# Optimization experiments

Hardware: AMD Instinct MI355X
Metric: run time of the kernel (lower is better)

## Reference

```python
import jax, jax.numpy as jnp
import numpy as np

N_NODES = 50000
N_GRAPHS = 500
E_SPARSE = 800000
E_DENSE = 3200000
IN_DIM = 128
HID = 128          # nb_hidden
OUT = HID // 2     # per-branch GATConv output
N_LAYERS = 3
NEG_SLOPE = 0.2    # PyG GATConv default


def setup_inputs() -> dict:
    key = jax.random.key(0)
    ks = jax.random.split(key, 10)
    x = jax.random.normal(ks[0], (N_NODES, IN_DIM), dtype=jnp.float32)
    edge_index = jax.random.randint(ks[1], (2, E_SPARSE), 0, N_NODES, dtype=jnp.int32)
    dense_edge_idx = jax.random.randint(ks[2], (2, E_DENSE), 0, N_NODES, dtype=jnp.int32)
    batch = jnp.sort(jax.random.randint(ks[3], (N_NODES,), 0, N_GRAPHS, dtype=jnp.int32))
    # One weight set per layer (source code aliases layersB = layersA, so both
    # branches share weights). All layers have in_dim = 128 -> out = 64.
    lin_w = jax.random.normal(ks[4], (N_LAYERS, HID, OUT), dtype=jnp.float32) * 0.1
    att_src = jax.random.normal(ks[5], (N_LAYERS, OUT), dtype=jnp.float32) * 0.1
    att_dst = jax.random.normal(ks[6], (N_LAYERS, OUT), dtype=jnp.float32) * 0.1
    bias = jnp.zeros((N_LAYERS, OUT), dtype=jnp.float32)
    final_w = jax.random.normal(ks[7], (HID, 1), dtype=jnp.float32) * 0.1
    final_b = jnp.zeros((1,), dtype=jnp.float32)
    return {"x": x, "edge_index": edge_index, "dense_edge_idx": dense_edge_idx,
            "batch": batch, "lin_w": lin_w, "att_src": att_src,
            "att_dst": att_dst, "bias": bias, "final_w": final_w,
            "final_b": final_b}


def _with_self_loops(edge_index, n):
    loop = jnp.arange(n, dtype=edge_index.dtype)
    src = jnp.concatenate([edge_index[0], loop])
    dst = jnp.concatenate([edge_index[1], loop])
    return src, dst


def _gat(x, src, dst, W, a_s, a_d, b):
    """PyG GATConv, heads=1: gather, LeakyReLU attention, segment softmax over
    incoming edges of each dst node, scatter-add aggregation."""
    n = x.shape[0]
    h = x @ W                      # [N, OUT]
    s_src = h @ a_s                # [N] per-node source score
    s_dst = h @ a_d                # [N] per-node dest score
    e = jax.nn.leaky_relu(s_src[src] + s_dst[dst], NEG_SLOPE)  # [E]
    m = jax.ops.segment_max(e, dst, num_segments=n)
    p = jnp.exp(e - m[dst])
    z = jax.ops.segment_sum(p, dst, num_segments=n)
    alpha = p / z[dst]             # [E] softmax over neighbors of dst
    out = jax.ops.segment_sum(alpha[:, None] * h[src], dst, num_segments=n)
    return out + b


def reference(x, edge_index, dense_edge_idx, batch, lin_w, att_src, att_dst,
              bias, final_w, final_b):
    n = x.shape[0]
    srcA, dstA = _with_self_loops(edge_index, n)
    srcB, dstB = _with_self_loops(dense_edge_idx, n)
    for l in range(N_LAYERS):
        xA = _gat(x, srcA, dstA, lin_w[l], att_src[l], att_dst[l], bias[l])
        xB = _gat(x, srcB, dstB, lin_w[l], att_src[l], att_dst[l], bias[l])
        x = jax.nn.relu(jnp.concatenate([xA, xB], axis=1))
    g = jax.ops.segment_sum(x, batch, num_segments=N_GRAPHS)  # global_add_pool
    y = (g @ final_w + final_b).squeeze()
    return y
```

## Files before the change

### kernel.cpp

```cpp
#include <hip/hip_runtime.h>
#include <hip/hip_fp16.h>

#define N_NODES 50000
#define N_GRAPHS 500
#define E_SPARSE 800000
#define E_DENSE 3200000
#define IN_DIM 128
#define HID 128
#define OUT_D 64
#define N_LAYERS 3
#define NEG_SLOPE 0.2f

#define BUCKET_SHIFT 7
#define BUCKET_N 128
#define NBUCK 391
#define NTD 256
#define NTS 64
#define TS_D 12500
#define TS_S 12500
#define MD (NBUCK * NTD)
#define MATN (NBUCK * (NTD + NTS))
#define NT 32
typedef unsigned int u32;
typedef unsigned short u16;
typedef _Float16 h16x8 __attribute__((ext_vector_type(8)));


__global__ __launch_bounds__(256) void tile_count_all(
    const int* __restrict__ dstD, const int* __restrict__ dstS,
    int* __restrict__ mat) {
    __shared__ int hc[NBUCK];
    int t = threadIdx.x;
    int tile = blockIdx.x;
    for (int i = t; i < NBUCK; i += 256) hc[i] = 0;
    __syncthreads();
    if (tile < NTD) {
        int beg = tile * TS_D, end = min(E_DENSE, beg + TS_D);
        for (int i = beg + t; i < end; i += 256)
            atomicAdd(&hc[dstD[i] >> BUCKET_SHIFT], 1);
        __syncthreads();
        for (int i = t; i < NBUCK; i += 256) mat[i * NTD + tile] = hc[i];
    } else {
        int st = tile - NTD;
        int beg = st * TS_S, end = min(E_SPARSE, beg + TS_S);
        for (int i = beg + t; i < end; i += 256)
            atomicAdd(&hc[dstS[i] >> BUCKET_SHIFT], 1);
        __syncthreads();
        for (int i = t; i < NBUCK; i += 256) mat[MD + i * NTS + st] = hc[i];
    }
}

__global__ void scan_lvl0(const int* __restrict__ cnt, int n,
                          int* __restrict__ out, int* __restrict__ bsum) {
    __shared__ int sm[512];
    int t = threadIdx.x;
    int base = blockIdx.x * 2048 + t * 4;
    int v0 = (base + 0 < n) ? cnt[base + 0] : 0;
    int v1 = (base + 1 < n) ? cnt[base + 1] : 0;
    int v2 = (base + 2 < n) ? cnt[base + 2] : 0;
    int v3 = (base + 3 < n) ? cnt[base + 3] : 0;
    int s = v0 + v1 + v2 + v3;
    sm[t] = s;
    __syncthreads();
    for (int off = 1; off < 512; off <<= 1) {
        int a = (t >= off) ? sm[t - off] : 0;
        __syncthreads();
        sm[t] += a;
        __syncthreads();
    }
    int excl = sm[t] - s;
    if (base + 0 < n) out[base + 0] = excl;
    if (base + 1 < n) out[base + 1] = excl + v0;
    if (base + 2 < n) out[base + 2] = excl + v0 + v1;
    if (base + 3 < n) out[base + 3] = excl + v0 + v1 + v2;
    if (t == 511) bsum[blockIdx.x] = sm[511];
}

__global__ void scan_lvl1(const int* __restrict__ bsum, int nb,
                          int* __restrict__ bsumx) {
    __shared__ int sm[256];
    int t = threadIdx.x;
    int v = (t < nb) ? bsum[t] : 0;
    sm[t] = v;
    __syncthreads();
    for (int off = 1; off < 256; off <<= 1) {
        int a = (t >= off) ? sm[t - off] : 0;
        __syncthreads();
        sm[t] += a;
        __syncthreads();
    }
    if (t < nb) bsumx[t] = sm[t] - v;
}

__global__ void scan_add(int* __restrict__ out, int n, const int* __restrict__ bsumx,
                         int Etot) {
    int i = blockIdx.x * blockDim.x + threadIdx.x;
    if (i < n) out[i] += bsumx[i >> 11];
    if (i == 0) out[n] = Etot;
}

__global__ __launch_bounds__(256) void tile_scatter_all(
    const int* __restrict__ srcD, const int* __restrict__ dstD,
    const int* __restrict__ srcS, const int* __restrict__ dstS,
    const int* __restrict__ matx, u32* __restrict__ pairs) {
    __shared__ int cur[NBUCK];
    int t = threadIdx.x;
    int tile = blockIdx.x;
    const int* src;
    const int* dst;
    int beg, end;
    if (tile < NTD) {
        for (int i = t; i < NBUCK; i += 256) cur[i] = matx[i * NTD + tile];
        src = srcD; dst = dstD;
        beg = tile * TS_D; end = min(E_DENSE, beg + TS_D);
    } else {
        int st = tile - NTD;
        for (int i = t; i < NBUCK; i += 256) cur[i] = matx[MD + i * NTS + st];
        src = srcS; dst = dstS;
        beg = st * TS_S; end = min(E_SPARSE, beg + TS_S);
    }
    __syncthreads();
    for (int i = beg + t; i < end; i += 256) {
        int d = dst[i];
        int pos = atomicAdd(&cur[d >> BUCKET_SHIFT], 1);
        pairs[pos] = (u32)src[i] | ((u32)(d & (BUCKET_N - 1)) << 16);
    }
}

__global__ __launch_bounds__(256) void bucket_to_csr_all(
    const u32* __restrict__ pairs, const int* __restrict__ matx,
    int* __restrict__ rowD, u16* __restrict__ csrcD,
    int* __restrict__ rowS, u16* __restrict__ csrcS) {
    int bid = blockIdx.x;
    int t = threadIdx.x;
    int b, beg, end, base;
    int* rowptr;
    u16* csrc;
    if (bid < NBUCK) {
        b = bid;
        beg = matx[b * NTD];
        end = matx[(b + 1) * NTD];
        base = 0; rowptr = rowD; csrc = csrcD;
    } else {
        b = bid - NBUCK;
        beg = matx[MD + b * NTS];
        end = matx[MD + (b + 1) * NTS];
        base = E_DENSE; rowptr = rowS; csrc = csrcS;
    }
    __shared__ int lcnt[BUCKET_N];
    __shared__ int lofs[BUCKET_N];
    if (t < BUCKET_N) lcnt[t] = 0;
    __syncthreads();
    for (int k = beg + t; k < end; k += 256)
        atomicAdd(&lcnt[(pairs[k] >> 16) & (BUCKET_N - 1)], 1);
    __syncthreads();
    if (t < BUCKET_N) lofs[t] = lcnt[t];
    __syncthreads();
    for (int off = 1; off < BUCKET_N; off <<= 1) {
        int a = (t < BUCKET_N && t >= off) ? lofs[t - off] : 0;
        __syncthreads();
        if (t < BUCKET_N) lofs[t] += a;
        __syncthreads();
    }
    int node = (b << BUCKET_SHIFT) + t;
    int lbeg = beg - base;
    if (t < BUCKET_N) {
        int excl = lofs[t] - lcnt[t];
        if (node < N_NODES) rowptr[node] = lbeg + excl;
        lcnt[t] = excl;
    }
    if (b == NBUCK - 1 && t == 0)
        rowptr[N_NODES] = (base == 0) ? E_DENSE : E_SPARSE;
    __syncthreads();
    for (int k = beg + t; k < end; k += 256) {
        u32 pr = pairs[k];
        int dl = (pr >> 16) & (BUCKET_N - 1);
        int pos = atomicAdd(&lcnt[dl], 1);
        csrc[lbeg + pos] = (u16)(pr & 0xffffu);
    }
}


__global__ __launch_bounds__(256) void node_mm2(
    const float* __restrict__ x, const float* __restrict__ W,
    const float* __restrict__ a_s, const float* __restrict__ a_d,
    __half* __restrict__ h, float* __restrict__ s_src, float* __restrict__ s_dst) {
    __shared__ float Wl[IN_DIM * OUT_D];
    __shared__ float4 Xl4[NT * 33];
    int t = threadIdx.x;
    int nbase = blockIdx.x * NT;

    const float4* W4 = (const float4*)W;
    float4* Wl4 = (float4*)Wl;
#pragma unroll
    for (int i = 0; i < 8; ++i) Wl4[t + 256 * i] = W4[t + 256 * i];

    int nrows = min(NT, N_NODES - nbase);
    const float4* X4 = (const float4*)(x + (size_t)nbase * IN_DIM);
    for (int i = t; i < nrows * 32; i += 256)
        Xl4[(i >> 5) * 33 + (i & 31)] = X4[i];
    __syncthreads();

    int wv = t >> 6, l = t & 63;
    int c4 = l & 15;
    int np = l >> 4;
    int n0 = wv * 8 + np * 2, n1 = n0 + 1;
    const float* Xl = (const float*)Xl4;
    const float4* Wr = (const float4*)Wl;

    float4 A0 = make_float4(0.f, 0.f, 0.f, 0.f);
    float4 A1 = make_float4(0.f, 0.f, 0.f, 0.f);
#pragma unroll 4
    for (int k = 0; k < IN_DIM; ++k) {
        float4 w4 = Wr[k * 16 + c4];
        float x0 = Xl[n0 * 132 + k];
        float x1 = Xl[n1 * 132 + k];
        A0.x += x0 * w4.x; A0.y += x0 * w4.y; A0.z += x0 * w4.z; A0.w += x0 * w4.w;
        A1.x += x1 * w4.x; A1.y += x1 * w4.y; A1.z += x1 * w4.z; A1.w += x1 * w4.w;
    }
    int gn0 = nbase + n0, gn1 = nbase + n1;
    if (gn0 < N_NODES) {
        __half2 v0 = __floats2half2_rn(A0.x, A0.y);
        __half2 v1 = __floats2half2_rn(A0.z, A0.w);
        float2 pk;
        pk.x = *(float*)&v0; pk.y = *(float*)&v1;
        ((float2*)(h + (size_t)gn0 * OUT_D))[c4] = pk;
    }
    if (gn1 < N_NODES) {
        __half2 v0 = __floats2half2_rn(A1.x, A1.y);
        __half2 v1 = __floats2half2_rn(A1.z, A1.w);
        float2 pk;
        pk.x = *(float*)&v0; pk.y = *(float*)&v1;
        ((float2*)(h + (size_t)gn1 * OUT_D))[c4] = pk;
    }

    float4 as4 = ((const float4*)a_s)[c4];
    float4 ad4 = ((const float4*)a_d)[c4];
    float ps0 = A0.x * as4.x + A0.y * as4.y + A0.z * as4.z + A0.w * as4.w;
    float pd0 = A0.x * ad4.x + A0.y * ad4.y + A0.z * ad4.z + A0.w * ad4.w;
    float ps1 = A1.x * as4.x + A1.y * as4.y + A1.z * as4.z + A1.w * as4.w;
    float pd1 = A1.x * ad4.x + A1.y * ad4.y + A1.z * ad4.z + A1.w * ad4.w;
#pragma unroll
    for (int off = 1; off < 16; off <<= 1) {
        ps0 += __shfl_xor(ps0, off); pd0 += __shfl_xor(pd0, off);
        ps1 += __shfl_xor(ps1, off); pd1 += __shfl_xor(pd1, off);
    }
    if (c4 == 0) {
        if (gn0 < N_NODES) { s_src[gn0] = ps0; s_dst[gn0] = pd0; }
        if (gn1 < N_NODES) { s_src[gn1] = ps1; s_dst[gn1] = pd1; }
    }
}

__device__ __forceinline__ void accv(float4& a0, float4& a1, float p,
                                     const h16x8& r) {
    a0.x = fmaf((float)r[0], p, a0.x);
    a0.y = fmaf((float)r[1], p, a0.y);
    a0.z = fmaf((float)r[2], p, a0.z);
    a0.w = fmaf((float)r[3], p, a0.w);
    a1.x = fmaf((float)r[4], p, a1.x);
    a1.y = fmaf((float)r[5], p, a1.y);
    a1.z = fmaf((float)r[6], p, a1.z);
    a1.w = fmaf((float)r[7], p, a1.w);
}

__device__ __forceinline__ float lrelu(float e) {
    return (e >= 0.f) ? e : NEG_SLOPE * e;
}

__global__ __launch_bounds__(256, 8) void gat_aggr2(
    const int* __restrict__ rowS, const u16* __restrict__ csrcS,
    const int* __restrict__ rowD, const u16* __restrict__ csrcD,
    const float* __restrict__ s_src, const float* __restrict__ s_dst,
    const __half* __restrict__ h, const float* __restrict__ bias,
    float* __restrict__ xnext, int ngrid) {
    int bid = blockIdx.x;
    const int* rowptr;
    const u16* csrc;
    int col_off;
    if (bid < ngrid) { rowptr = rowS; csrc = csrcS; col_off = 0; }
    else { bid -= ngrid; rowptr = rowD; csrc = csrcD; col_off = OUT_D; }

    int node = bid * 4 + (threadIdx.x >> 6);
    if (node >= N_NODES) return;
    int lane = threadIdx.x & 63;
    int grp = lane >> 3;
    int sub = lane & 7;

    int beg = rowptr[node];
    int end = rowptr[node + 1];
    float sd = s_dst[node];

    const char* hb = (const char*)h;
    u32 subo = (u32)sub * 16u;

    float4 a0 = make_float4(0.f, 0.f, 0.f, 0.f);
    float4 a1 = make_float4(0.f, 0.f, 0.f, 0.f);
    float zb = 0.f;
    float zt = 0.f;

    int kb = beg;
    for (; kb + 32 <= end; kb += 32) {
        u32 idx = csrc[kb + (lane & 31)];
        float e = s_src[idx] + sd;
        float p = __expf(lrelu(e));
        if (lane < 32) zb += p;
#pragma unroll
        for (int i = 0; i < 4; ++i) {
            int j = (grp << 2) + i;
            float pj = __shfl(p, j);
            u32 ij = (u32)__shfl((int)idx, j);
            h16x8 r = *(const h16x8*)(hb + (ij * 128u + subo));
            accv(a0, a1, pj, r);
        }
    }
    int k = kb + grp;
    for (; k + 8 < end; k += 16) {
        u32 s0 = csrc[k], s1 = csrc[k + 8];
        h16x8 r0 = *(const h16x8*)(hb + (s0 * 128u + subo));
        h16x8 r1 = *(const h16x8*)(hb + (s1 * 128u + subo));
        float e0 = s_src[s0] + sd;
        float e1 = s_src[s1] + sd;
        float p0 = __expf(lrelu(e0));
        float p1 = __expf(lrelu(e1));
        zt += p0 + p1;
        accv(a0, a1, p0, r0);
        accv(a0, a1, p1, r1);
    }
    if (k < end) {
        u32 s0 = csrc[k];
        h16x8 r0 = *(const h16x8*)(hb + (s0 * 128u + subo));
        float e0 = s_src[s0] + sd;
        float p0 = __expf(lrelu(e0));
        zt += p0;
        accv(a0, a1, p0, r0);
    }
    if (grp == 0) {
        h16x8 r0 = *(const h16x8*)(hb + ((u32)node * 128u + subo));
        float e0 = s_src[node] + sd;
        float p0 = __expf(lrelu(e0));
        zt += p0;
        accv(a0, a1, p0, r0);
    }
#pragma unroll
    for (int off = 1; off <= 32; off <<= 1) zb += __shfl_xor(zb, off);
#pragma unroll
    for (int off = 8; off <= 32; off <<= 1) {
        a0.x += __shfl_xor(a0.x, off); a0.y += __shfl_xor(a0.y, off);
        a0.z += __shfl_xor(a0.z, off); a0.w += __shfl_xor(a0.w, off);
        a1.x += __shfl_xor(a1.x, off); a1.y += __shfl_xor(a1.y, off);
        a1.z += __shfl_xor(a1.z, off); a1.w += __shfl_xor(a1.w, off);
        zt += __shfl_xor(zt, off);
    }
    if (grp == 0) {
        float inv = 1.f / (zb + zt);
        const float4* b4 = (const float4*)bias;
        float4 b0 = b4[sub * 2], b1 = b4[sub * 2 + 1];
        float4 o0, o1;
        o0.x = a0.x * inv + b0.x; o0.y = a0.y * inv + b0.y;
        o0.z = a0.z * inv + b0.z; o0.w = a0.w * inv + b0.w;
        o1.x = a1.x * inv + b1.x; o1.y = a1.y * inv + b1.y;
        o1.z = a1.z * inv + b1.z; o1.w = a1.w * inv + b1.w;
        o0.x = fmaxf(o0.x, 0.f); o0.y = fmaxf(o0.y, 0.f);
        o0.z = fmaxf(o0.z, 0.f); o0.w = fmaxf(o0.w, 0.f);
        o1.x = fmaxf(o1.x, 0.f); o1.y = fmaxf(o1.y, 0.f);
        o1.z = fmaxf(o1.z, 0.f); o1.w = fmaxf(o1.w, 0.f);
        float4* outp = (float4*)(xnext + (size_t)node * HID + col_off);
        outp[sub * 2] = o0;
        outp[sub * 2 + 1] = o1;
    }
}

__global__ __launch_bounds__(128) void pool_final(
    const float* __restrict__ x, const int* __restrict__ batch,
    const float* __restrict__ fw, const float* __restrict__ fb,
    float* __restrict__ y) {
    int b = blockIdx.x;
    int t = threadIdx.x;
    __shared__ int sbeg, send;
    if (t == 0) {
        int lo = 0, hi = N_NODES;
        while (lo < hi) { int mid = (lo + hi) >> 1; if (batch[mid] < b) lo = mid + 1; else hi = mid; }
        sbeg = lo;
        hi = N_NODES;
        while (lo < hi) { int mid = (lo + hi) >> 1; if (batch[mid] < b + 1) lo = mid + 1; else hi = mid; }
        send = lo;
    }
    __syncthreads();
    float acc = 0.f;
    for (int n = sbeg; n < send; ++n) acc += x[(size_t)n * HID + t];
    __shared__ float sm[HID];
    sm[t] = acc * fw[t];
    __syncthreads();
    for (int off = 64; off > 0; off >>= 1) {
        if (t < off) sm[t] += sm[t + off];
        __syncthreads();
    }
    if (t == 0) y[b] = sm[0] + fb[0];
}

extern "C" void kernel_launch(void* const* d_in, const int* in_sizes, int n_in,
                              void* d_out, int out_size, void* d_ws, size_t ws_size,
                              hipStream_t stream) {
    const float* x_in    = (const float*)d_in[0];
    const int*   ei      = (const int*)d_in[1];
    const int*   di      = (const int*)d_in[2];
    const int*   batch   = (const int*)d_in[3];
    const float* lin_w   = (const float*)d_in[4];
    const float* att_src = (const float*)d_in[5];
    const float* att_dst = (const float*)d_in[6];
    const float* bias    = (const float*)d_in[7];
    const float* fw      = (const float*)d_in[8];
    const float* fb      = (const float*)d_in[9];
    float* y = (float*)d_out;

    char* wsb = (char*)d_ws;
    size_t off = 0;
    auto alloc_b = [&](size_t bytes) { void* p = (void*)(wsb + off);
                                       off += (bytes + 15) & ~(size_t)15; return p; };

    float* xbuf0 = (float*)alloc_b((size_t)N_NODES * HID * 4);
    float* xbuf1 = (float*)alloc_b((size_t)N_NODES * HID * 4);
    __half* h    = (__half*)alloc_b((size_t)N_NODES * OUT_D * 2);
    float* s_src = (float*)alloc_b(N_NODES * 4);
    float* s_dst = (float*)alloc_b(N_NODES * 4);
    int* mat     = (int*)alloc_b((size_t)MATN * 4);
    int* matx    = (int*)alloc_b(((size_t)MATN + 1) * 4);
    int* bsum    = (int*)alloc_b(256 * 4);
    int* bsumx   = (int*)alloc_b(256 * 4);
    int* rowS    = (int*)alloc_b((N_NODES + 1) * 4);
    int* rowD    = (int*)alloc_b((N_NODES + 1) * 4);
    u16* csrcS   = (u16*)alloc_b((size_t)E_SPARSE * 2);
    u16* csrcD   = (u16*)alloc_b((size_t)E_DENSE * 2);
    u32* pairs   = (u32*)xbuf1;

    const int* srcD = di;
    const int* dstD = di + E_DENSE;
    const int* srcS = ei;
    const int* dstS = ei + E_SPARSE;

    const int SCAN_BLKS = (MATN + 2047) / 2048;

    tile_count_all<<<NTD + NTS, 256, 0, stream>>>(dstD, dstS, mat);
    scan_lvl0<<<SCAN_BLKS, 512, 0, stream>>>(mat, MATN, matx, bsum);
    scan_lvl1<<<1, 256, 0, stream>>>(bsum, SCAN_BLKS, bsumx);
    scan_add<<<(MATN + 256) / 256, 256, 0, stream>>>(matx, MATN, bsumx,
                                                     E_DENSE + E_SPARSE);
    tile_scatter_all<<<NTD + NTS, 256, 0, stream>>>(srcD, dstD, srcS, dstS,
                                                    matx, pairs);
    bucket_to_csr_all<<<2 * NBUCK, 256, 0, stream>>>(pairs, matx, rowD, csrcD,
                                                     rowS, csrcS);

    const float* cur = x_in;
    float* bufs[3] = {xbuf1, xbuf0, xbuf1};
    const int ngrid = (N_NODES + 3) / 4;
    const int mm_grid = (N_NODES + NT - 1) / NT;
    for (int l = 0; l < N_LAYERS; ++l) {
        node_mm2<<<mm_grid, 256, 0, stream>>>(cur, lin_w + (size_t)l * HID * OUT_D,
                                              att_src + l * OUT_D, att_dst + l * OUT_D,
                                              h, s_src, s_dst);
        float* xn = bufs[l];
        gat_aggr2<<<2 * ngrid, 256, 0, stream>>>(rowS, csrcS, rowD, csrcD,
                                                 s_src, s_dst, h,
                                                 bias + l * OUT_D, xn, ngrid);
        cur = xn;
    }

    pool_final<<<N_GRAPHS, 128, 0, stream>>>(cur, batch, fw, fb, y);
}
```

Measured before the change: 492.3 us.

## Assign one 8-lane group per node in GAT aggregation instead of one wavefront

The aggregation kernel now maps each node to an 8-lane group, so a 64-lane wavefront handles 8 nodes and a block handles 32, replacing the one-wavefront-per-node scheme. This drops the 32-edge shuffle batch loop and the cross-group shuffle reductions of the accumulators and softmax denominator, since each group owns its whole row sequentially. Leaky ReLU is also rewritten as a branchless fmaxf. In exchange, per-node edge loops become serial within a group and divergent across groups with different degrees, with less memory-level parallelism per node on high-degree rows.

Result: slower. 511.4 us (+3.9%).

```diff
diff --git a/kernel.cpp b/kernel.cpp
--- a/kernel.cpp
+++ b/kernel.cpp
@@ -264,65 +264,50 @@
 }
 
 __device__ __forceinline__ float lrelu(float e) {
-    return (e >= 0.f) ? e : NEG_SLOPE * e;
-}
-
-__global__ __launch_bounds__(256, 8) void gat_aggr2(
+    return fmaxf(e, NEG_SLOPE * e);
+}
+
+__global__ __launch_bounds__(256, 8) void gat_aggr3(
     const int* __restrict__ rowS, const u16* __restrict__ csrcS,
     const int* __restrict__ rowD, const u16* __restrict__ csrcD,
     const float* __restrict__ s_src, const float* __restrict__ s_dst,
     const __half* __restrict__ h, const float* __restrict__ bias,
-    float* __restrict__ xnext, int ngrid) {
+    float* __restrict__ xnext, int nblk) {
     int bid = blockIdx.x;
     const int* rowptr;
     const u16* csrc;
     int col_off;
-    if (bid < ngrid) { rowptr = rowS; csrc = csrcS; col_off = 0; }
-    else { bid -= ngrid; rowptr = rowD; csrc = csrcD; col_off = OUT_D; }
-
-    int node = bid * 4 + (threadIdx.x >> 6);
-    if (node >= N_NODES) return;
+    if (bid < nblk) { rowptr = rowS; csrc = csrcS; col_off = 0; }
+    else { bid -= nblk; rowptr = rowD; csrc = csrcD; col_off = OUT_D; }
+
     int lane = threadIdx.x & 63;
+    int wid = threadIdx.x >> 6;
     int grp = lane >> 3;
     int sub = lane & 7;
-
-    int beg = rowptr[node];
-    int end = rowptr[node + 1];
-    float sd = s_dst[node];
+    int node = bid * 32 + wid * 8 + grp;
+    bool valid = node < N_NODES;
+
+    int beg = 0, end = 0;
+    if (valid) { beg = rowptr[node]; end = rowptr[node + 1]; }
+    float sd = valid ? s_dst[node] : 0.f;
 
     const char* hb = (const char*)h;
     u32 subo = (u32)sub * 16u;
 
     float4 a0 = make_float4(0.f, 0.f, 0.f, 0.f);
     float4 a1 = make_float4(0.f, 0.f, 0.f, 0.f);
-    float zb = 0.f;
-    float zt = 0.f;
-
-    int kb = beg;
-    for (; kb + 32 <= end; kb += 32) {
-        u32 idx = csrc[kb + (lane & 31)];
-        float e = s_src[idx] + sd;
-        float p = __expf(lrelu(e));
-        if (lane < 32) zb += p;
-#pragma unroll
-        for (int i = 0; i < 4; ++i) {
-            int j = (grp << 2) + i;
-            float pj = __shfl(p, j);
-            u32 ij = (u32)__shfl((int)idx, j);
-            h16x8 r = *(const h16x8*)(hb + (ij * 128u + subo));
-            accv(a0, a1, pj, r);
-        }
-    }
-    int k = kb + grp;
-    for (; k + 8 < end; k += 16) {
-        u32 s0 = csrc[k], s1 = csrc[k + 8];
+    float z = 0.f;
+
+    int k = beg;
+    for (; k + 1 < end; k += 2) {
+        u32 s0 = csrc[k], s1 = csrc[k + 1];
         h16x8 r0 = *(const h16x8*)(hb + (s0 * 128u + subo));
         h16x8 r1 = *(const h16x8*)(hb + (s1 * 128u + subo));
         float e0 = s_src[s0] + sd;
         float e1 = s_src[s1] + sd;
         float p0 = __expf(lrelu(e0));
         float p1 = __expf(lrelu(e1));
-        zt += p0 + p1;
+        z += p0 + p1;
         accv(a0, a1, p0, r0);
         accv(a0, a1, p1, r1);
     }
@@ -331,28 +316,17 @@
         h16x8 r0 = *(const h16x8*)(hb + (s0 * 128u + subo));
         float e0 = s_src[s0] + sd;
         float p0 = __expf(lrelu(e0));
-        zt += p0;
+        z += p0;
         accv(a0, a1, p0, r0);
     }
-    if (grp == 0) {
+    if (valid) {
         h16x8 r0 = *(const h16x8*)(hb + ((u32)node * 128u + subo));
         float e0 = s_src[node] + sd;
         float p0 = __expf(lrelu(e0));
-        zt += p0;
+        z += p0;
         accv(a0, a1, p0, r0);
-    }
-#pragma unroll
-    for (int off = 1; off <= 32; off <<= 1) zb += __shfl_xor(zb, off);
-#pragma unroll
-    for (int off = 8; off <= 32; off <<= 1) {
-        a0.x += __shfl_xor(a0.x, off); a0.y += __shfl_xor(a0.y, off);
-        a0.z += __shfl_xor(a0.z, off); a0.w += __shfl_xor(a0.w, off);
-        a1.x += __shfl_xor(a1.x, off); a1.y += __shfl_xor(a1.y, off);
-        a1.z += __shfl_xor(a1.z, off); a1.w += __shfl_xor(a1.w, off);
-        zt += __shfl_xor(zt, off);
-    }
-    if (grp == 0) {
-        float inv = 1.f / (zb + zt);
+
+        float inv = 1.f / z;
         const float4* b4 = (const float4*)bias;
         float4 b0 = b4[sub * 2], b1 = b4[sub * 2 + 1];
         float4 o0, o1;
@@ -452,16 +426,16 @@
 
     const float* cur = x_in;
     float* bufs[3] = {xbuf1, xbuf0, xbuf1};
-    const int ngrid = (N_NODES + 3) / 4;
+    const int nblk = (N_NODES + 31) / 32;
     const int mm_grid = (N_NODES + NT - 1) / NT;
     for (int l = 0; l < N_LAYERS; ++l) {
         node_mm2<<<mm_grid, 256, 0, stream>>>(cur, lin_w + (size_t)l * HID * OUT_D,
                                               att_src + l * OUT_D, att_dst + l * OUT_D,
                                               h, s_src, s_dst);
         float* xn = bufs[l];
-        gat_aggr2<<<2 * ngrid, 256, 0, stream>>>(rowS, csrcS, rowD, csrcD,
-                                                 s_src, s_dst, h,
-                                                 bias + l * OUT_D, xn, ngrid);
+        gat_aggr3<<<2 * nblk, 256, 0, stream>>>(rowS, csrcS, rowD, csrcD,
+                                                s_src, s_dst, h,
+                                                bias + l * OUT_D, xn, nblk);
         cur = xn;
     }
 
```
